# Kernel tuning notes

Measured on AMD Instinct MI355X. Metric: run time of the kernel, lower is better.

The kernel has to match this reference:

```python
import jax, jax.numpy as jnp
import numpy as np
import math

WS = 8       # window_size
NH = 4       # num_heads
D = 256      # d_model
B = 16
HH = 64
WW = 64
EPS = 1e-5


def _sincos_pe(ws, d):
    pe = np.zeros((ws * ws, d), np.float32)
    dh = d // 2
    y = np.repeat(np.arange(ws), ws).astype(np.float32)
    x = np.tile(np.arange(ws), ws).astype(np.float32)
    div = np.exp(np.arange(0, dh, 2).astype(np.float32) * (-math.log(10000.0) / dh))
    pe[:, 0:dh:2] = np.sin(y[:, None] * div)
    pe[:, 1:dh:2] = np.cos(y[:, None] * div)
    pe[:, dh::2] = np.sin(x[:, None] * div)
    pe[:, dh + 1::2] = np.cos(x[:, None] * div)
    return jnp.asarray(pe)[None]  # [1, ws*ws, d]


def setup_inputs() -> dict:
    key = jax.random.key(0)
    ks = iter(jax.random.split(key, 32))
    rnd = lambda *s: jax.random.normal(next(ks), s, dtype=jnp.float32) * 0.02
    inp = {
        'feat_A': jax.random.normal(next(ks), (B, HH * WW, D), dtype=jnp.float32),
        'feat_B': jax.random.normal(next(ks), (B, HH * WW, D), dtype=jnp.float32),
        'local_pe': _sincos_pe(WS, D),
    }
    for s in ('A', 'B'):
        inp[f'qkv_w_{s}'] = rnd(3, D, D)
        inp[f'qkv_b_{s}'] = rnd(3, D)
        inp[f'out_w_{s}'] = rnd(D, D)
        inp[f'out_b_{s}'] = rnd(D)
        inp[f'norm_g_{s}'] = jnp.ones((D,), jnp.float32)
        inp[f'norm_b_{s}'] = jnp.zeros((D,), jnp.float32)
        inp[f'ffn_norm_g_{s}'] = jnp.ones((D,), jnp.float32)
        inp[f'ffn_norm_b_{s}'] = jnp.zeros((D,), jnp.float32)
        inp[f'ffn_w1_{s}'] = rnd(2 * D, D)
        inp[f'ffn_b1_{s}'] = rnd(2 * D)
        inp[f'ffn_w2_{s}'] = rnd(D, 2 * D)
        inp[f'ffn_b2_{s}'] = rnd(D)
    inp['H'] = HH
    inp['W'] = WW
    return inp


def _partition(x, H, W):
    # [B, H*W, C] -> [B*nW, WS*WS, C]; H, W assumed divisible by WS (no pad branch)
    b, _, c = x.shape
    x = x.reshape(b, H // WS, WS, W // WS, WS, c)
    return x.transpose(0, 1, 3, 2, 4, 5).reshape(-1, WS * WS, c)


def _reverse(w, b, H, W):
    c = w.shape[-1]
    x = w.reshape(b, H // WS, W // WS, WS, WS, c)
    return x.transpose(0, 1, 3, 2, 4, 5).reshape(b, H * W, c)


def _ln(x, g, b):
    m = jnp.mean(x, -1, keepdims=True)
    v = jnp.mean(jnp.square(x - m), -1, keepdims=True)
    return (x - m) * jax.lax.rsqrt(v + EPS) * g + b


def _mha(q_in, kv_in, qkv_w, qkv_b, out_w, out_b):
    s, c = q_in.shape[1], q_in.shape[2]
    dh = c // NH
    q = (q_in @ qkv_w[0].T + qkv_b[0]).reshape(-1, s, NH, dh)
    k = (kv_in @ qkv_w[1].T + qkv_b[1]).reshape(-1, s, NH, dh)
    v = (kv_in @ qkv_w[2].T + qkv_b[2]).reshape(-1, s, NH, dh)
    attn = jax.nn.softmax(jnp.einsum('bqhd,bkhd->bhqk', q, k) / math.sqrt(dh), axis=-1)
    o = jnp.einsum('bhqk,bkhd->bqhd', attn, v).reshape(-1, s, c)
    return o @ out_w.T + out_b


def _ffn(x, w1, b1, w2, b2):
    return jax.nn.gelu(x @ w1.T + b1, approximate=False) @ w2.T + b2


def reference(feat_A, feat_B, local_pe,
              qkv_w_A, qkv_b_A, out_w_A, out_b_A,
              qkv_w_B, qkv_b_B, out_w_B, out_b_B,
              norm_g_A, norm_b_A, ffn_norm_g_A, ffn_norm_b_A,
              ffn_w1_A, ffn_b1_A, ffn_w2_A, ffn_b2_A,
              norm_g_B, norm_b_B, ffn_norm_g_B, ffn_norm_b_B,
              ffn_w1_B, ffn_b1_B, ffn_w2_B, ffn_b2_B,
              H, W):
    b = feat_A.shape[0]
    sc_A, sc_B = feat_A, feat_B
    win_A = _partition(feat_A, H, W) + local_pe
    win_B = _partition(feat_B, H, W) + local_pe
    attn_A = _mha(win_A, win_B, qkv_w_A, qkv_b_A, out_w_A, out_b_A)
    attn_B = _mha(win_B, win_A, qkv_w_B, qkv_b_B, out_w_B, out_b_B)
    fA = _reverse(attn_A, b, H, W)
    fB = _reverse(attn_B, b, H, W)
    fA = _ln(fA + sc_A, norm_g_A, norm_b_A)
    fA = _ln(fA + _ffn(fA, ffn_w1_A, ffn_b1_A, ffn_w2_A, ffn_b2_A), ffn_norm_g_A, ffn_norm_b_A)
    fB = _ln(fB + sc_B, norm_g_B, norm_b_B)
    fB = _ln(fB + _ffn(fB, ffn_w1_B, ffn_b1_B, ffn_w2_B, ffn_b2_B), ffn_norm_g_B, ffn_norm_b_B)
    return (fA, fB)
```

## Files before the change

### kernel.cpp

```cpp
#include <hip/hip_runtime.h>
#include <hip/hip_bf16.h>
#include <math.h>

typedef __bf16 bf16;
typedef __bf16 bf16x8 __attribute__((ext_vector_type(8)));
typedef __bf16 bf16x4 __attribute__((ext_vector_type(4)));
typedef float f32x4 __attribute__((ext_vector_type(4)));

#define NTOK 65536
#define DMODEL 256

#define GL16(g, l) __builtin_amdgcn_global_load_lds( \
    (const __attribute__((address_space(1))) void*)(g), \
    (__attribute__((address_space(3))) void*)(l), 16, 0, 0)

__device__ __forceinline__ int unwin_idx(int m) {
    int widx = m >> 6, t = m & 63;
    int b = widx >> 6, wl = widx & 63;
    return (b << 12) | (((wl >> 3) * 8 + (t >> 3)) << 6) | ((wl & 7) * 8 + (t & 7));
}

__device__ __forceinline__ float gelu_fast(float x) {
    float z = 0.7978845608f * (x + 0.044715f * x * x * x);
    float e = __expf(2.f * z);
    float t = (e - 1.f) / (e + 1.f);
    return 0.5f * x * (1.f + t);
}

__global__ __launch_bounds__(256)
void prep_win(const float* __restrict__ fA, const float* __restrict__ fB,
              const float* __restrict__ pe,
              bf16* __restrict__ awA, bf16* __restrict__ awB)
{
    const float* f = blockIdx.y ? fB : fA;
    bf16* aw = blockIdx.y ? awB : awA;
    int m = blockIdx.x * 8 + (threadIdx.x >> 5);
    int c = (threadIdx.x & 31) * 8;
    int g = unwin_idx(m), t = m & 63;
    const float4* fs = reinterpret_cast<const float4*>(f + (size_t)g * 256 + c);
    const float4* ps = reinterpret_cast<const float4*>(pe + t * 256 + c);
    float4 a0 = fs[0], a1 = fs[1], p0 = ps[0], p1 = ps[1];
    bf16x8 o;
    o[0] = (bf16)(a0.x + p0.x); o[1] = (bf16)(a0.y + p0.y);
    o[2] = (bf16)(a0.z + p0.z); o[3] = (bf16)(a0.w + p0.w);
    o[4] = (bf16)(a1.x + p1.x); o[5] = (bf16)(a1.y + p1.y);
    o[6] = (bf16)(a1.z + p1.z); o[7] = (bf16)(a1.w + p1.w);
    *reinterpret_cast<bf16x8*>(aw + (size_t)m * 256 + c) = o;
}

__global__ __launch_bounds__(256)
void cvt8(const float* __restrict__ s0, const float* __restrict__ s1,
          const float* __restrict__ s2, const float* __restrict__ s3,
          const float* __restrict__ s4, const float* __restrict__ s5,
          const float* __restrict__ s6, const float* __restrict__ s7,
          bf16* __restrict__ d)
{
    int idx = (blockIdx.x * 256 + threadIdx.x) * 4;
    const float* s; int off;
    if      (idx < 196608) { s = s0; off = 0; }
    else if (idx < 262144) { s = s1; off = 196608; }
    else if (idx < 393216) { s = s2; off = 262144; }
    else if (idx < 524288) { s = s3; off = 393216; }
    else if (idx < 720896) { s = s4; off = 524288; }
    else if (idx < 786432) { s = s5; off = 720896; }
    else if (idx < 917504) { s = s6; off = 786432; }
    else                   { s = s7; off = 917504; }
    float4 v = *reinterpret_cast<const float4*>(s + (idx - off));
    bf16x4 o; o[0] = (bf16)v.x; o[1] = (bf16)v.y; o[2] = (bf16)v.z; o[3] = (bf16)v.w;
    *reinterpret_cast<bf16x4*>(d + idx) = o;
}

__global__ __launch_bounds__(256, 4)
void gemm_qkv2(const bf16* __restrict__ awA, const bf16* __restrict__ awB,
               const bf16* __restrict__ wA, const bf16* __restrict__ wB,
               const float* __restrict__ bA, const float* __restrict__ bB,
               bf16* __restrict__ qA, bf16* __restrict__ kA, bf16* __restrict__ vA,
               bf16* __restrict__ qB, bf16* __restrict__ kB, bf16* __restrict__ vB)
{
    __shared__ bf16 As[2][4096];
    __shared__ bf16 Bs[2][4096];
    const int tid = threadIdx.x;
    const int bx = blockIdx.x;
    const int xcd = bx & 7, slot = bx >> 3;
    const int L = xcd * 768 + slot;
    const int mt = L / 6, nb = L - mt * 6;
    const int pass = mt >> 9, mb = mt & 511;
    const int seg = nb >> 1, nl0 = (nb & 1) * 128;
    const int m0 = mb * 128;

    const bf16* A = pass ? awB : awA;
    const bf16* Wf = (seg == 0) ? (pass ? wB : wA) : (pass ? wA : wB);
    const float* Bf = (seg == 0) ? (pass ? bB : bA) : (pass ? bA : bB);
    const bf16* W = Wf + (size_t)seg * 65536;
    const float* bia = Bf + seg * 256;
    bf16* qout = pass ? qB : qA;
    bf16* kout = pass ? kA : kB;
    bf16* vout = pass ? vA : vB;

    const int lane = tid & 63, w = tid >> 6;
    const int wr = w >> 1, wc = w & 1;
    const int lr = lane & 15, lg = lane >> 4;
    const int srow = tid >> 2, scol = (tid & 3) * 8;

    const bf16* Ag = A + (size_t)(m0 + srow) * 256 + scol;
    const bf16* Bg = W + (size_t)(nl0 + srow) * 256 + scol;

    f32x4 acc[4][4];
    const f32x4 zero = {0.f, 0.f, 0.f, 0.f};
#pragma unroll
    for (int mi = 0; mi < 4; ++mi)
#pragma unroll
        for (int nj = 0; nj < 4; ++nj) acc[mi][nj] = zero;

    auto stage = [&](int buf, int k0) {
        GL16(Ag + k0, &As[buf][tid * 8]);
        GL16(Ag + 64 * 256 + k0, &As[buf][2048 + tid * 8]);
        GL16(Bg + k0, &Bs[buf][tid * 8]);
        GL16(Bg + 64 * 256 + k0, &Bs[buf][2048 + tid * 8]);
    };
    auto compute = [&](int buf) {
        bf16x8 af[4], bfr[4];
#pragma unroll
        for (int mi = 0; mi < 4; ++mi)
            af[mi] = *reinterpret_cast<const bf16x8*>(&As[buf][(wr * 64 + mi * 16 + lr) * 32 + lg * 8]);
#pragma unroll
        for (int nj = 0; nj < 4; ++nj)
            bfr[nj] = *reinterpret_cast<const bf16x8*>(&Bs[buf][(wc * 64 + nj * 16 + lr) * 32 + lg * 8]);
#pragma unroll
        for (int mi = 0; mi < 4; ++mi)
#pragma unroll
            for (int nj = 0; nj < 4; ++nj)
                acc[mi][nj] = __builtin_amdgcn_mfma_f32_16x16x32_bf16(af[mi], bfr[nj], acc[mi][nj], 0, 0, 0);
    };

    stage(0, 0);
    __syncthreads();
#pragma unroll
    for (int t = 0; t < 7; ++t) {
        stage((t + 1) & 1, (t + 1) * 32);
        compute(t & 1);
        __syncthreads();
    }
    compute(1);

    if (seg == 2) {
        const int widx = mb * 2 + wr;
#pragma unroll
        for (int nj = 0; nj < 4; ++nj) {
            int cl = nl0 + wc * 64 + nj * 16 + lr;
            float bv = bia[cl];
#pragma unroll
            for (int mi = 0; mi < 4; ++mi) {
                bf16x4 o;
#pragma unroll
                for (int i = 0; i < 4; ++i) o[i] = (bf16)(acc[mi][nj][i] + bv);
                *reinterpret_cast<bf16x4*>(vout + ((size_t)widx * 256 + cl) * 64 + mi * 16 + lg * 4) = o;
            }
        }
    } else {
        bf16* out = (seg == 0) ? qout : kout;
#pragma unroll
        for (int nj = 0; nj < 4; ++nj) {
            int cl = nl0 + wc * 64 + nj * 16 + lr;
            float bv = bia[cl];
#pragma unroll
            for (int mi = 0; mi < 4; ++mi)
#pragma unroll
                for (int i = 0; i < 4; ++i) {
                    int row = m0 + wr * 64 + mi * 16 + lg * 4 + i;
                    out[(size_t)row * 256 + cl] = (bf16)(acc[mi][nj][i] + bv);
                }
        }
    }
}

__global__ __launch_bounds__(256, 4)
void gemm_gelu(const bf16* __restrict__ y1A, const bf16* __restrict__ y1B,
               const bf16* __restrict__ wA, const bf16* __restrict__ wB,
               const float* __restrict__ bA, const float* __restrict__ bB,
               bf16* __restrict__ hbA, bf16* __restrict__ hbB)
{
    __shared__ bf16 lds[17408];
    bf16* As = lds;
    bf16* Bs = lds + 8192;
    const int tid = threadIdx.x;
    const int bx = blockIdx.x;
    const int xcd = bx & 7, slot = bx >> 3;
    const int L = xcd * 512 + slot;
    const int mt = L >> 2, nb = L & 3;
    const int str = mt >> 9, mb = mt & 511;
    const int m0 = mb * 128, n0 = nb * 128;

    const bf16* A = str ? y1B : y1A;
    const bf16* W = str ? wB : wA;
    const float* bia = str ? bB : bA;
    bf16* C = str ? hbB : hbA;

    const int lane = tid & 63, w = tid >> 6;
    const int wr = w >> 1, wc = w & 1;
    const int lr = lane & 15, lg = lane >> 4;
    const int srow = tid >> 2, scol = (tid & 3) * 8;

    const bf16* Ag = A + (size_t)(m0 + srow) * 256 + scol;
    const bf16* Bg = W + (size_t)(n0 + srow) * 256 + scol;

    f32x4 acc[4][4];
    const f32x4 zero = {0.f, 0.f, 0.f, 0.f};
#pragma unroll
    for (int mi = 0; mi < 4; ++mi)
#pragma unroll
        for (int nj = 0; nj < 4; ++nj) acc[mi][nj] = zero;

    auto stage = [&](int buf, int k0) {
        GL16(Ag + k0, &As[buf * 4096 + tid * 8]);
        GL16(Ag + 64 * 256 + k0, &As[buf * 4096 + 2048 + tid * 8]);
        GL16(Bg + k0, &Bs[buf * 4096 + tid * 8]);
        GL16(Bg + 64 * 256 + k0, &Bs[buf * 4096 + 2048 + tid * 8]);
    };
    auto compute = [&](int buf) {
        bf16x8 af[4], bfr[4];
#pragma unroll
        for (int mi = 0; mi < 4; ++mi)
            af[mi] = *reinterpret_cast<const bf16x8*>(&As[buf * 4096 + (wr * 64 + mi * 16 + lr) * 32 + lg * 8]);
#pragma unroll
        for (int nj = 0; nj < 4; ++nj)
            bfr[nj] = *reinterpret_cast<const bf16x8*>(&Bs[buf * 4096 + (wc * 64 + nj * 16 + lr) * 32 + lg * 8]);
#pragma unroll
        for (int mi = 0; mi < 4; ++mi)
#pragma unroll
            for (int nj = 0; nj < 4; ++nj)
                acc[mi][nj] = __builtin_amdgcn_mfma_f32_16x16x32_bf16(af[mi], bfr[nj], acc[mi][nj], 0, 0, 0);
    };

    stage(0, 0);
    __syncthreads();
#pragma unroll
    for (int t = 0; t < 7; ++t) {
        stage((t + 1) & 1, (t + 1) * 32);
        compute(t & 1);
        __syncthreads();
    }
    compute(1);

    __syncthreads();
#pragma unroll
    for (int nj = 0; nj < 4; ++nj) {
        int coll = wc * 64 + nj * 16 + lr;
        float bv = bia[n0 + coll];
#pragma unroll
        for (int mi = 0; mi < 4; ++mi)
#pragma unroll
            for (int i = 0; i < 4; ++i) {
                int rowl = wr * 64 + mi * 16 + lg * 4 + i;
                lds[rowl * 136 + coll] = (bf16)gelu_fast(acc[mi][nj][i] + bv);
            }
    }
    __syncthreads();
#pragma unroll
    for (int j = 0; j < 4; ++j)
#pragma unroll
        for (int h = 0; h < 2; ++h) {
            int rowl = j * 32 + (tid >> 3);
            int coll = h * 64 + (tid & 7) * 8;
            *reinterpret_cast<bf16x8*>(C + (size_t)(m0 + rowl) * 512 + n0 + coll) =
                *reinterpret_cast<const bf16x8*>(&lds[rowl * 136 + coll]);
        }
}

template<int WK, int UNWIN>
__global__ __launch_bounds__(256, 4)
void gemm_out(const bf16* __restrict__ A0, const bf16* __restrict__ A1,
              const bf16* __restrict__ W0, const bf16* __restrict__ W1,
              const float* __restrict__ b0, const float* __restrict__ b1,
              bf16* __restrict__ C0, bf16* __restrict__ C1)
{
    __shared__ bf16 lds[17408];
    bf16* As = lds;
    bf16* Bs = lds + 8192;
    const int tid = threadIdx.x;
    const int bx = blockIdx.x;
    const int xcd = bx & 7, slot = bx >> 3;
    const int L = xcd * 256 + slot;
    const int mt = L >> 1, nb = L & 1;
    const int str = mt >> 9, mb = mt & 511;
    const int m0 = mb * 128, n0 = nb * 128;

    const bf16* A = str ? A1 : A0;
    const bf16* W = str ? W1 : W0;
    const float* bia = str ? b1 : b0;
    bf16* C = str ? C1 : C0;

    const int lane = tid & 63, w = tid >> 6;
    const int wr = w >> 1, wc = w & 1;
    const int lr = lane & 15, lg = lane >> 4;
    const int srow = tid >> 2, scol = (tid & 3) * 8;

    const bf16* Ag = A + (size_t)(m0 + srow) * WK + scol;
    const bf16* Bg = W + (size_t)(n0 + srow) * WK + scol;

    f32x4 acc[4][4];
    const f32x4 zero = {0.f, 0.f, 0.f, 0.f};
#pragma unroll
    for (int mi = 0; mi < 4; ++mi)
#pragma unroll
        for (int nj = 0; nj < 4; ++nj) acc[mi][nj] = zero;

    auto stage = [&](int buf, int k0) {
        GL16(Ag + k0, &As[buf * 4096 + tid * 8]);
        GL16(Ag + (size_t)64 * WK + k0, &As[buf * 4096 + 2048 + tid * 8]);
        GL16(Bg + k0, &Bs[buf * 4096 + tid * 8]);
        GL16(Bg + (size_t)64 * WK + k0, &Bs[buf * 4096 + 2048 + tid * 8]);
    };
    auto compute = [&](int buf) {
        bf16x8 af[4], bfr[4];
#pragma unroll
        for (int mi = 0; mi < 4; ++mi)
            af[mi] = *reinterpret_cast<const bf16x8*>(&As[buf * 4096 + (wr * 64 + mi * 16 + lr) * 32 + lg * 8]);
#pragma unroll
        for (int nj = 0; nj < 4; ++nj)
            bfr[nj] = *reinterpret_cast<const bf16x8*>(&Bs[buf * 4096 + (wc * 64 + nj * 16 + lr) * 32 + lg * 8]);
#pragma unroll
        for (int mi = 0; mi < 4; ++mi)
#pragma unroll
            for (int nj = 0; nj < 4; ++nj)
                acc[mi][nj] = __builtin_amdgcn_mfma_f32_16x16x32_bf16(af[mi], bfr[nj], acc[mi][nj], 0, 0, 0);
    };

    const int NT = WK / 32;
    stage(0, 0);
    __syncthreads();
#pragma unroll
    for (int t = 0; t < NT - 1; ++t) {
        stage((t + 1) & 1, (t + 1) * 32);
        compute(t & 1);
        __syncthreads();
    }
    compute((NT - 1) & 1);

    __syncthreads();
#pragma unroll
    for (int nj = 0; nj < 4; ++nj) {
        int coll = wc * 64 + nj * 16 + lr;
        float bv = bia[n0 + coll];
#pragma unroll
        for (int mi = 0; mi < 4; ++mi)
#pragma unroll
            for (int i = 0; i < 4; ++i) {
                int rowl = wr * 64 + mi * 16 + lg * 4 + i;
                lds[rowl * 136 + coll] = (bf16)(acc[mi][nj][i] + bv);
            }
    }
    __syncthreads();
#pragma unroll
    for (int j = 0; j < 4; ++j) {
        int rowl = j * 32 + (tid >> 3);
        int gr = UNWIN ? unwin_idx(m0 + rowl) : (m0 + rowl);
#pragma unroll
        for (int h = 0; h < 2; ++h) {
            int coll = h * 64 + (tid & 7) * 8;
            *reinterpret_cast<bf16x8*>(C + (size_t)gr * 256 + n0 + coll) =
                *reinterpret_cast<const bf16x8*>(&lds[rowl * 136 + coll]);
        }
    }
}

template<int RESF, int OUTF>
__global__ __launch_bounds__(256)
void ln_fz(const bf16* __restrict__ x0, const bf16* __restrict__ x1,
           const float* __restrict__ rf0, const float* __restrict__ rf1,
           const bf16* __restrict__ rb0, const bf16* __restrict__ rb1,
           const float* __restrict__ g0, const float* __restrict__ g1,
           const float* __restrict__ be0, const float* __restrict__ be1,
           float* __restrict__ of0, float* __restrict__ of1,
           bf16* __restrict__ ob0, bf16* __restrict__ ob1)
{
    const int bx = blockIdx.x;
    const int str = bx >> 14, b = bx & 16383;
    const bf16* x = str ? x1 : x0;
    const float* rf = str ? rf1 : rf0;
    const bf16* rb = str ? rb1 : rb0;
    const float* gamma = str ? g1 : g0;
    const float* beta = str ? be1 : be0;
    float* outf = str ? of1 : of0;
    bf16* outb = str ? ob1 : ob0;

    int row = b * 4 + (threadIdx.x >> 6);
    int lane = threadIdx.x & 63;
    size_t base = (size_t)row * 256 + lane * 4;
    bf16x4 xv = *reinterpret_cast<const bf16x4*>(x + base);
    float v[4];
    if (RESF) {
        float4 rv = *reinterpret_cast<const float4*>(rf + base);
        v[0] = rv.x + (float)xv[0];
        v[1] = rv.y + (float)xv[1];
        v[2] = rv.z + (float)xv[2];
        v[3] = rv.w + (float)xv[3];
    } else {
        bf16x4 rv = *reinterpret_cast<const bf16x4*>(rb + base);
        v[0] = (float)rv[0] + (float)xv[0];
        v[1] = (float)rv[1] + (float)xv[1];
        v[2] = (float)rv[2] + (float)xv[2];
        v[3] = (float)rv[3] + (float)xv[3];
    }
    float s = v[0] + v[1] + v[2] + v[3];
    float q = v[0] * v[0] + v[1] * v[1] + v[2] * v[2] + v[3] * v[3];
#pragma unroll
    for (int m = 1; m < 64; m <<= 1) {
        s += __shfl_xor(s, m);
        q += __shfl_xor(q, m);
    }
    float mean = s * (1.f / 256.f);
    float var = q * (1.f / 256.f) - mean * mean;
    float rstd = rsqrtf(var + 1e-5f);
    float4 gv = *reinterpret_cast<const float4*>(gamma + lane * 4);
    float4 bv = *reinterpret_cast<const float4*>(beta + lane * 4);
    float o[4];
    o[0] = (v[0] - mean) * rstd * gv.x + bv.x;
    o[1] = (v[1] - mean) * rstd * gv.y + bv.y;
    o[2] = (v[2] - mean) * rstd * gv.z + bv.z;
    o[3] = (v[3] - mean) * rstd * gv.w + bv.w;
    if (OUTF) {
        float4 ov; ov.x = o[0]; ov.y = o[1]; ov.z = o[2]; ov.w = o[3];
        *reinterpret_cast<float4*>(outf + base) = ov;
    } else {
        bf16x4 ob;
        ob[0] = (bf16)o[0]; ob[1] = (bf16)o[1]; ob[2] = (bf16)o[2]; ob[3] = (bf16)o[3];
        *reinterpret_cast<bf16x4*>(outb + base) = ob;
    }
}

__global__ __launch_bounds__(256)
void attn_win2(const bf16* qA, const bf16* __restrict__ kA,
               const bf16* __restrict__ vA,
               const bf16* qB, const bf16* __restrict__ kB,
               const bf16* __restrict__ vB)
{
    __shared__ bf16 Ps[4][64][72];
    const int tid = threadIdx.x;
    const int wv = tid >> 6, lane = tid & 63;
    const int str = blockIdx.x >> 10, widx = blockIdx.x & 1023, head = wv;
    const int lr = lane & 15, lg = lane >> 4;
    const bf16* qbuf = str ? qB : qA;
    const bf16* kbuf = str ? kB : kA;
    const bf16* vtbuf = str ? vB : vA;
    bf16* obuf = const_cast<bf16*>(qbuf);
    const bf16* qb = qbuf + (size_t)widx * 64 * 256 + head * 64;
    const bf16* kb = kbuf + (size_t)widx * 64 * 256 + head * 64;
    const bf16* vb = vtbuf + (size_t)widx * 16384 + head * 64 * 64;

    const f32x4 zero = {0.f, 0.f, 0.f, 0.f};
    f32x4 sacc[4][4];
#pragma unroll
    for (int mi = 0; mi < 4; ++mi)
#pragma unroll
        for (int nj = 0; nj < 4; ++nj) sacc[mi][nj] = zero;

#pragma unroll
    for (int k0 = 0; k0 < 64; k0 += 32) {
        bf16x8 af[4], bfr[4];
#pragma unroll
        for (int mi = 0; mi < 4; ++mi)
            af[mi] = *reinterpret_cast<const bf16x8*>(qb + (size_t)(mi * 16 + lr) * 256 + k0 + lg * 8);
#pragma unroll
        for (int nj = 0; nj < 4; ++nj)
            bfr[nj] = *reinterpret_cast<const bf16x8*>(kb + (size_t)(nj * 16 + lr) * 256 + k0 + lg * 8);
#pragma unroll
        for (int mi = 0; mi < 4; ++mi)
#pragma unroll
            for (int nj = 0; nj < 4; ++nj)
                sacc[mi][nj] = __builtin_amdgcn_mfma_f32_16x16x32_bf16(af[mi], bfr[nj], sacc[mi][nj], 0, 0, 0);
    }

    const float c = 0.125f * 1.4426950408889634f;
    float rsum[4][4];
#pragma unroll
    for (int mi = 0; mi < 4; ++mi)
#pragma unroll
        for (int i = 0; i < 4; ++i) {
            float m = fmaxf(fmaxf(sacc[mi][0][i], sacc[mi][1][i]), fmaxf(sacc[mi][2][i], sacc[mi][3][i]));
            m = fmaxf(m, __shfl_xor(m, 1));
            m = fmaxf(m, __shfl_xor(m, 2));
            m = fmaxf(m, __shfl_xor(m, 4));
            m = fmaxf(m, __shfl_xor(m, 8));
#pragma unroll
            for (int nj = 0; nj < 4; ++nj)
                sacc[mi][nj][i] = exp2f((sacc[mi][nj][i] - m) * c);
            float s = sacc[mi][0][i] + sacc[mi][1][i] + sacc[mi][2][i] + sacc[mi][3][i];
            s += __shfl_xor(s, 1);
            s += __shfl_xor(s, 2);
            s += __shfl_xor(s, 4);
            s += __shfl_xor(s, 8);
            rsum[mi][i] = s;
        }

#pragma unroll
    for (int mi = 0; mi < 4; ++mi)
#pragma unroll
        for (int nj = 0; nj < 4; ++nj)
#pragma unroll
            for (int i = 0; i < 4; ++i)
                Ps[wv][mi * 16 + lg * 4 + i][nj * 16 + lr] = (bf16)sacc[mi][nj][i];

    f32x4 oacc[4][4];
#pragma unroll
    for (int mi = 0; mi < 4; ++mi)
#pragma unroll
        for (int nj = 0; nj < 4; ++nj) oacc[mi][nj] = zero;
#pragma unroll
    for (int k0 = 0; k0 < 64; k0 += 32) {
        bf16x8 af[4], bfr[4];
#pragma unroll
        for (int mi = 0; mi < 4; ++mi)
            af[mi] = *reinterpret_cast<const bf16x8*>(&Ps[wv][mi * 16 + lr][k0 + lg * 8]);
#pragma unroll
        for (int nj = 0; nj < 4; ++nj)
            bfr[nj] = *reinterpret_cast<const bf16x8*>(vb + (size_t)(nj * 16 + lr) * 64 + k0 + lg * 8);
#pragma unroll
        for (int mi = 0; mi < 4; ++mi)
#pragma unroll
            for (int nj = 0; nj < 4; ++nj)
                oacc[mi][nj] = __builtin_amdgcn_mfma_f32_16x16x32_bf16(af[mi], bfr[nj], oacc[mi][nj], 0, 0, 0);
    }
#pragma unroll
    for (int mi = 0; mi < 4; ++mi)
#pragma unroll
        for (int i = 0; i < 4; ++i) {
            float inv = 1.0f / rsum[mi][i];
            int row = mi * 16 + lg * 4 + i;
#pragma unroll
            for (int nj = 0; nj < 4; ++nj)
                obuf[((size_t)widx * 64 + row) * 256 + head * 64 + nj * 16 + lr] =
                    (bf16)(oacc[mi][nj][i] * inv);
        }
}

extern "C" void kernel_launch(void* const* d_in, const int* in_sizes, int n_in,
                              void* d_out, int out_size, void* d_ws, size_t ws_size,
                              hipStream_t stream)
{
    const float* feat_A       = (const float*)d_in[0];
    const float* feat_B       = (const float*)d_in[1];
    const float* pe           = (const float*)d_in[2];
    const float* qkv_w_A      = (const float*)d_in[3];
    const float* qkv_b_A      = (const float*)d_in[4];
    const float* out_w_A      = (const float*)d_in[5];
    const float* out_b_A      = (const float*)d_in[6];
    const float* norm_g_A     = (const float*)d_in[7];
    const float* norm_b_A     = (const float*)d_in[8];
    const float* ffn_norm_g_A = (const float*)d_in[9];
    const float* ffn_norm_b_A = (const float*)d_in[10];
    const float* ffn_w1_A     = (const float*)d_in[11];
    const float* ffn_b1_A     = (const float*)d_in[12];
    const float* ffn_w2_A     = (const float*)d_in[13];
    const float* ffn_b2_A     = (const float*)d_in[14];
    const float* qkv_w_B      = (const float*)d_in[15];
    const float* qkv_b_B      = (const float*)d_in[16];
    const float* out_w_B      = (const float*)d_in[17];
    const float* out_b_B      = (const float*)d_in[18];
    const float* norm_g_B     = (const float*)d_in[19];
    const float* norm_b_B     = (const float*)d_in[20];
    const float* ffn_norm_g_B = (const float*)d_in[21];
    const float* ffn_norm_b_B = (const float*)d_in[22];
    const float* ffn_w1_B     = (const float*)d_in[23];
    const float* ffn_b1_B     = (const float*)d_in[24];
    const float* ffn_w2_B     = (const float*)d_in[25];
    const float* ffn_b2_B     = (const float*)d_in[26];

    char* ws = (char*)d_ws;
    const size_t BFE = (size_t)NTOK * 256;
    const size_t BFB = BFE * 2;

    bf16* Wb = (bf16*)ws;
    size_t off = 2u * 1024 * 1024;
    bf16* awA = (bf16*)(ws + off); off += BFB;
    bf16* awB = (bf16*)(ws + off); off += BFB;
    bf16* qA  = (bf16*)(ws + off); off += BFB;
    bf16* kA  = (bf16*)(ws + off); off += BFB;
    bf16* vA  = (bf16*)(ws + off); off += BFB;
    bf16* qB  = (bf16*)(ws + off); off += BFB;
    bf16* kB  = (bf16*)(ws + off); off += BFB;
    bf16* vB  = (bf16*)(ws + off); off += BFB;
    bf16* tb1A = kA;
    bf16* tb1B = vA;
    bf16* y1A = kB;
    bf16* y1B = vB;
    bf16* hbA = awA;
    bf16* hbB = kA;
    bf16* tb2A = qA;
    bf16* tb2B = qB;

    bf16* w_qkvA = Wb + 0;
    bf16* w_outA = Wb + 196608;
    bf16* w_f1A  = Wb + 262144;
    bf16* w_f2A  = Wb + 393216;
    bf16* w_qkvB = Wb + 524288;
    bf16* w_outB = Wb + 720896;
    bf16* w_f1B  = Wb + 786432;
    bf16* w_f2B  = Wb + 917504;

    cvt8<<<1024, 256, 0, stream>>>(qkv_w_A, out_w_A, ffn_w1_A, ffn_w2_A,
                                   qkv_w_B, out_w_B, ffn_w1_B, ffn_w2_B, Wb);
    prep_win<<<dim3(8192, 2), 256, 0, stream>>>(feat_A, feat_B, pe, awA, awB);

    gemm_qkv2<<<6144, 256, 0, stream>>>(awA, awB, w_qkvA, w_qkvB,
                                        qkv_b_A, qkv_b_B,
                                        qA, kA, vA, qB, kB, vB);

    attn_win2<<<2048, 256, 0, stream>>>(qA, kA, vA, qB, kB, vB);

    gemm_out<256, 1><<<2048, 256, 0, stream>>>(qA, qB, w_outA, w_outB,
                                               out_b_A, out_b_B, tb1A, tb1B);
    ln_fz<1, 0><<<32768, 256, 0, stream>>>(tb1A, tb1B, feat_A, feat_B,
                                           nullptr, nullptr,
                                           norm_g_A, norm_g_B, norm_b_A, norm_b_B,
                                           nullptr, nullptr, y1A, y1B);
    gemm_gelu<<<4096, 256, 0, stream>>>(y1A, y1B, w_f1A, w_f1B,
                                        ffn_b1_A, ffn_b1_B, hbA, hbB);
    gemm_out<512, 0><<<2048, 256, 0, stream>>>(hbA, hbB, w_f2A, w_f2B,
                                               ffn_b2_A, ffn_b2_B, tb2A, tb2B);
    ln_fz<0, 1><<<32768, 256, 0, stream>>>(tb2A, tb2B, nullptr, nullptr,
                                           y1A, y1B,
                                           ffn_norm_g_A, ffn_norm_g_B,
                                           ffn_norm_b_A, ffn_norm_b_B,
                                           (float*)d_out, (float*)d_out + BFE,
                                           nullptr, nullptr);
}
```

Baseline: 455.2 us.

## Fuse window partition and PE add into QKV GEMM A-load; stage Q/K stores via LDS

Removes the prep_win kernel and has the QKV GEMM read fp32 features directly, gather them through the window index, add the positional encoding and convert to bf16 while writing a padded LDS tile. This drops the intermediate bf16 window buffers, saving a full write and read of them. The fp32 A tile is now read six times, once per N-block, instead of the smaller bf16 copy, and the loads are synchronous rather than async global-to-LDS. Separately, Q/K outputs are staged through LDS so they can be written with coalesced 16-byte stores instead of scalar scattered bf16 stores.

```diff
diff --git a/kernel.cpp b/kernel.cpp
--- a/kernel.cpp
+++ b/kernel.cpp
@@ -25,27 +25,6 @@
     float e = __expf(2.f * z);
     float t = (e - 1.f) / (e + 1.f);
     return 0.5f * x * (1.f + t);
-}
-
-__global__ __launch_bounds__(256)
-void prep_win(const float* __restrict__ fA, const float* __restrict__ fB,
-              const float* __restrict__ pe,
-              bf16* __restrict__ awA, bf16* __restrict__ awB)
-{
-    const float* f = blockIdx.y ? fB : fA;
-    bf16* aw = blockIdx.y ? awB : awA;
-    int m = blockIdx.x * 8 + (threadIdx.x >> 5);
-    int c = (threadIdx.x & 31) * 8;
-    int g = unwin_idx(m), t = m & 63;
-    const float4* fs = reinterpret_cast<const float4*>(f + (size_t)g * 256 + c);
-    const float4* ps = reinterpret_cast<const float4*>(pe + t * 256 + c);
-    float4 a0 = fs[0], a1 = fs[1], p0 = ps[0], p1 = ps[1];
-    bf16x8 o;
-    o[0] = (bf16)(a0.x + p0.x); o[1] = (bf16)(a0.y + p0.y);
-    o[2] = (bf16)(a0.z + p0.z); o[3] = (bf16)(a0.w + p0.w);
-    o[4] = (bf16)(a1.x + p1.x); o[5] = (bf16)(a1.y + p1.y);
-    o[6] = (bf16)(a1.z + p1.z); o[7] = (bf16)(a1.w + p1.w);
-    *reinterpret_cast<bf16x8*>(aw + (size_t)m * 256 + c) = o;
 }
 
 __global__ __launch_bounds__(256)
@@ -71,14 +50,16 @@
 }
 
 __global__ __launch_bounds__(256, 4)
-void gemm_qkv2(const bf16* __restrict__ awA, const bf16* __restrict__ awB,
+void gemm_qkvf(const float* __restrict__ feat_A, const float* __restrict__ feat_B,
+               const float* __restrict__ pe,
                const bf16* __restrict__ wA, const bf16* __restrict__ wB,
                const float* __restrict__ bA, const float* __restrict__ bB,
                bf16* __restrict__ qA, bf16* __restrict__ kA, bf16* __restrict__ vA,
                bf16* __restrict__ qB, bf16* __restrict__ kB, bf16* __restrict__ vB)
 {
-    __shared__ bf16 As[2][4096];
-    __shared__ bf16 Bs[2][4096];
+    __shared__ bf16 lds[18432];
+    bf16* As = lds;
+    bf16* Bs = lds + 10240;
     const int tid = threadIdx.x;
     const int bx = blockIdx.x;
     const int xcd = bx & 7, slot = bx >> 3;
@@ -88,7 +69,7 @@
     const int seg = nb >> 1, nl0 = (nb & 1) * 128;
     const int m0 = mb * 128;
 
-    const bf16* A = pass ? awB : awA;
+    const float* feat = pass ? feat_B : feat_A;
     const bf16* Wf = (seg == 0) ? (pass ? wB : wA) : (pass ? wA : wB);
     const float* Bf = (seg == 0) ? (pass ? bB : bA) : (pass ? bA : bB);
     const bf16* W = Wf + (size_t)seg * 65536;
@@ -101,8 +82,14 @@
     const int wr = w >> 1, wc = w & 1;
     const int lr = lane & 15, lg = lane >> 4;
     const int srow = tid >> 2, scol = (tid & 3) * 8;
-
-    const bf16* Ag = A + (size_t)(m0 + srow) * 256 + scol;
+    const int r = tid >> 1, cs = (tid & 1) * 16;
+
+    const int mrow = m0 + r;
+    const int tA = mrow & 63;
+    const int gA = unwin_idx(mrow);
+    const float* fsrc = feat + (size_t)gA * DMODEL + cs;
+    const float* psrc = pe + tA * DMODEL + cs;
+
     const bf16* Bg = W + (size_t)(nl0 + srow) * 256 + scol;
 
     f32x4 acc[4][4];
@@ -112,20 +99,31 @@
 #pragma unroll
         for (int nj = 0; nj < 4; ++nj) acc[mi][nj] = zero;
 
-    auto stage = [&](int buf, int k0) {
-        GL16(Ag + k0, &As[buf][tid * 8]);
-        GL16(Ag + 64 * 256 + k0, &As[buf][2048 + tid * 8]);
-        GL16(Bg + k0, &Bs[buf][tid * 8]);
-        GL16(Bg + 64 * 256 + k0, &Bs[buf][2048 + tid * 8]);
+    auto stageB = [&](int buf, int k0) {
+        GL16(Bg + k0, &Bs[buf * 4096 + tid * 8]);
+        GL16(Bg + 64 * 256 + k0, &Bs[buf * 4096 + 2048 + tid * 8]);
+    };
+    auto stageA = [&](int buf, int k0) {
+        const float4* fs = reinterpret_cast<const float4*>(fsrc + k0);
+        const float4* ps = reinterpret_cast<const float4*>(psrc + k0);
+        bf16* dst = &As[buf * 5120 + r * 40 + cs];
+#pragma unroll
+        for (int q = 0; q < 4; ++q) {
+            float4 a = fs[q], p = ps[q];
+            dst[q * 4 + 0] = (bf16)(a.x + p.x);
+            dst[q * 4 + 1] = (bf16)(a.y + p.y);
+            dst[q * 4 + 2] = (bf16)(a.z + p.z);
+            dst[q * 4 + 3] = (bf16)(a.w + p.w);
+        }
     };
     auto compute = [&](int buf) {
         bf16x8 af[4], bfr[4];
 #pragma unroll
         for (int mi = 0; mi < 4; ++mi)
-            af[mi] = *reinterpret_cast<const bf16x8*>(&As[buf][(wr * 64 + mi * 16 + lr) * 32 + lg * 8]);
+            af[mi] = *reinterpret_cast<const bf16x8*>(&As[buf * 5120 + (wr * 64 + mi * 16 + lr) * 40 + lg * 8]);
 #pragma unroll
         for (int nj = 0; nj < 4; ++nj)
-            bfr[nj] = *reinterpret_cast<const bf16x8*>(&Bs[buf][(wc * 64 + nj * 16 + lr) * 32 + lg * 8]);
+            bfr[nj] = *reinterpret_cast<const bf16x8*>(&Bs[buf * 4096 + (wc * 64 + nj * 16 + lr) * 32 + lg * 8]);
 #pragma unroll
         for (int mi = 0; mi < 4; ++mi)
 #pragma unroll
@@ -133,11 +131,13 @@
                 acc[mi][nj] = __builtin_amdgcn_mfma_f32_16x16x32_bf16(af[mi], bfr[nj], acc[mi][nj], 0, 0, 0);
     };
 
-    stage(0, 0);
+    stageB(0, 0);
+    stageA(0, 0);
     __syncthreads();
 #pragma unroll
     for (int t = 0; t < 7; ++t) {
-        stage((t + 1) & 1, (t + 1) * 32);
+        stageB((t + 1) & 1, (t + 1) * 32);
+        stageA((t + 1) & 1, (t + 1) * 32);
         compute(t & 1);
         __syncthreads();
     }
@@ -159,17 +159,29 @@
         }
     } else {
         bf16* out = (seg == 0) ? qout : kout;
+        __syncthreads();
 #pragma unroll
         for (int nj = 0; nj < 4; ++nj) {
-            int cl = nl0 + wc * 64 + nj * 16 + lr;
-            float bv = bia[cl];
+            int coll = wc * 64 + nj * 16 + lr;
+            float bv = bia[nl0 + coll];
 #pragma unroll
             for (int mi = 0; mi < 4; ++mi)
 #pragma unroll
                 for (int i = 0; i < 4; ++i) {
-                    int row = m0 + wr * 64 + mi * 16 + lg * 4 + i;
-                    out[(size_t)row * 256 + cl] = (bf16)(acc[mi][nj][i] + bv);
+                    int rowl = wr * 64 + mi * 16 + lg * 4 + i;
+                    lds[rowl * 136 + coll] = (bf16)(acc[mi][nj][i] + bv);
                 }
+        }
+        __syncthreads();
+#pragma unroll
+        for (int j = 0; j < 4; ++j) {
+            int rowl = j * 32 + (tid >> 3);
+#pragma unroll
+            for (int h = 0; h < 2; ++h) {
+                int coll = h * 64 + (tid & 7) * 8;
+                *reinterpret_cast<bf16x8*>(out + (size_t)(m0 + rowl) * 256 + nl0 + coll) =
+                    *reinterpret_cast<const bf16x8*>(&lds[rowl * 136 + coll]);
+            }
         }
     }
 }
@@ -600,9 +612,8 @@
 
     cvt8<<<1024, 256, 0, stream>>>(qkv_w_A, out_w_A, ffn_w1_A, ffn_w2_A,
                                    qkv_w_B, out_w_B, ffn_w1_B, ffn_w2_B, Wb);
-    prep_win<<<dim3(8192, 2), 256, 0, stream>>>(feat_A, feat_B, pe, awA, awB);
-
-    gemm_qkv2<<<6144, 256, 0, stream>>>(awA, awB, w_qkvA, w_qkvB,
+
+    gemm_qkvf<<<6144, 256, 0, stream>>>(feat_A, feat_B, pe, w_qkvA, w_qkvB,
                                         qkv_b_A, qkv_b_B,
                                         qA, kA, vA, qB, kB, vB);
 
```

Measured after the change: 493.7 us. 8.5% more time.

## Fuse FFN up-projection, GELU and down-projection into one kernel

Applied to the files above, without the earlier changes.

Replaces the separate GELU GEMM and second FFN GEMM with a single kernel that computes each 128-column hidden chunk into LDS and immediately accumulates it into the down-projection. This removes writing and rereading the 512-wide hidden activation to global memory and one kernel launch. It uses 512-thread blocks with larger LDS, so each block holds more registers (two accumulator sets) and occupancy drops. W1 is reloaded per block and several extra barriers are added per chunk.

```diff
diff --git a/kernel.cpp b/kernel.cpp
--- a/kernel.cpp
+++ b/kernel.cpp
@@ -174,97 +174,153 @@
     }
 }
 
-__global__ __launch_bounds__(256, 4)
-void gemm_gelu(const bf16* __restrict__ y1A, const bf16* __restrict__ y1B,
-               const bf16* __restrict__ wA, const bf16* __restrict__ wB,
-               const float* __restrict__ bA, const float* __restrict__ bB,
-               bf16* __restrict__ hbA, bf16* __restrict__ hbB)
-{
-    __shared__ bf16 lds[17408];
-    bf16* As = lds;
-    bf16* Bs = lds + 8192;
+__global__ __launch_bounds__(512, 2)
+void gemm_ffn(const bf16* __restrict__ y1A, const bf16* __restrict__ y1B,
+              const bf16* __restrict__ w1A, const bf16* __restrict__ w1B,
+              const bf16* __restrict__ w2A, const bf16* __restrict__ w2B,
+              const float* __restrict__ b1A, const float* __restrict__ b1B,
+              const float* __restrict__ b2A, const float* __restrict__ b2B,
+              bf16* __restrict__ tb2A, bf16* __restrict__ tb2B)
+{
+    __shared__ bf16 lds[33792];
+    bf16* Hs = lds + 16384;
     const int tid = threadIdx.x;
     const int bx = blockIdx.x;
-    const int xcd = bx & 7, slot = bx >> 3;
-    const int L = xcd * 512 + slot;
-    const int mt = L >> 2, nb = L & 3;
-    const int str = mt >> 9, mb = mt & 511;
-    const int m0 = mb * 128, n0 = nb * 128;
-
-    const bf16* A = str ? y1B : y1A;
-    const bf16* W = str ? wB : wA;
-    const float* bia = str ? bB : bA;
-    bf16* C = str ? hbB : hbA;
-
-    const int lane = tid & 63, w = tid >> 6;
-    const int wr = w >> 1, wc = w & 1;
+    const int L = (bx & 7) * 128 + (bx >> 3);
+    const int str = L >> 9, mb = L & 511;
+    const int m0 = mb * 128;
+
+    const bf16* Y  = str ? y1B : y1A;
+    const bf16* W1 = str ? w1B : w1A;
+    const bf16* W2 = str ? w2B : w2A;
+    const float* b1 = str ? b1B : b1A;
+    const float* b2 = str ? b2B : b2A;
+    bf16* out = str ? tb2B : tb2A;
+
+    const int w = tid >> 6, lane = tid & 63;
+    const int wr = w >> 2, wc = w & 3;
     const int lr = lane & 15, lg = lane >> 4;
     const int srow = tid >> 2, scol = (tid & 3) * 8;
 
-    const bf16* Ag = A + (size_t)(m0 + srow) * 256 + scol;
-    const bf16* Bg = W + (size_t)(n0 + srow) * 256 + scol;
-
-    f32x4 acc[4][4];
+    const bf16* Yg  = Y + (size_t)(m0 + srow) * 256 + scol;
+    const bf16* W2g = W2 + (size_t)srow * 512 + scol;
+
+    f32x4 acc2[4][4];
     const f32x4 zero = {0.f, 0.f, 0.f, 0.f};
 #pragma unroll
     for (int mi = 0; mi < 4; ++mi)
 #pragma unroll
-        for (int nj = 0; nj < 4; ++nj) acc[mi][nj] = zero;
-
-    auto stage = [&](int buf, int k0) {
-        GL16(Ag + k0, &As[buf * 4096 + tid * 8]);
-        GL16(Ag + 64 * 256 + k0, &As[buf * 4096 + 2048 + tid * 8]);
-        GL16(Bg + k0, &Bs[buf * 4096 + tid * 8]);
-        GL16(Bg + 64 * 256 + k0, &Bs[buf * 4096 + 2048 + tid * 8]);
-    };
-    auto compute = [&](int buf) {
-        bf16x8 af[4], bfr[4];
-#pragma unroll
-        for (int mi = 0; mi < 4; ++mi)
-            af[mi] = *reinterpret_cast<const bf16x8*>(&As[buf * 4096 + (wr * 64 + mi * 16 + lr) * 32 + lg * 8]);
-#pragma unroll
-        for (int nj = 0; nj < 4; ++nj)
-            bfr[nj] = *reinterpret_cast<const bf16x8*>(&Bs[buf * 4096 + (wc * 64 + nj * 16 + lr) * 32 + lg * 8]);
-#pragma unroll
-        for (int mi = 0; mi < 4; ++mi)
+        for (int nj = 0; nj < 4; ++nj) acc2[mi][nj] = zero;
+
+    for (int nb = 0; nb < 4; ++nb) {
+        const bf16* W1g = W1 + (size_t)(nb * 128 + srow) * 256 + scol;
+        f32x4 acc1[4][2];
+#pragma unroll
+        for (int mi = 0; mi < 4; ++mi)
+#pragma unroll
+            for (int nj = 0; nj < 2; ++nj) acc1[mi][nj] = zero;
+
+        auto stage1 = [&](int buf, int k0) {
+            GL16(Yg + k0,  &lds[buf * 4096 + tid * 8]);
+            GL16(W1g + k0, &lds[8192 + buf * 4096 + tid * 8]);
+        };
+        auto compute1 = [&](int buf) {
+            bf16x8 af[4], bfr[2];
+#pragma unroll
+            for (int mi = 0; mi < 4; ++mi)
+                af[mi] = *reinterpret_cast<const bf16x8*>(&lds[buf * 4096 + (wr * 64 + mi * 16 + lr) * 32 + lg * 8]);
+#pragma unroll
+            for (int nj = 0; nj < 2; ++nj)
+                bfr[nj] = *reinterpret_cast<const bf16x8*>(&lds[8192 + buf * 4096 + (wc * 32 + nj * 16 + lr) * 32 + lg * 8]);
+#pragma unroll
+            for (int mi = 0; mi < 4; ++mi)
+#pragma unroll
+                for (int nj = 0; nj < 2; ++nj)
+                    acc1[mi][nj] = __builtin_amdgcn_mfma_f32_16x16x32_bf16(af[mi], bfr[nj], acc1[mi][nj], 0, 0, 0);
+        };
+
+        stage1(0, 0);
+        __syncthreads();
+#pragma unroll
+        for (int t = 0; t < 7; ++t) {
+            stage1((t + 1) & 1, (t + 1) * 32);
+            compute1(t & 1);
+            __syncthreads();
+        }
+        compute1(1);
+
+#pragma unroll
+        for (int nj = 0; nj < 2; ++nj) {
+            int col = wc * 32 + nj * 16 + lr;
+            float bv = b1[nb * 128 + col];
+#pragma unroll
+            for (int mi = 0; mi < 4; ++mi)
+#pragma unroll
+                for (int i = 0; i < 4; ++i) {
+                    int row = wr * 64 + mi * 16 + lg * 4 + i;
+                    Hs[row * 136 + col] = (bf16)gelu_fast(acc1[mi][nj][i] + bv);
+                }
+        }
+        __syncthreads();
+
+        auto stage2 = [&](int buf, int k0) {
+            GL16(W2g + nb * 128 + k0, &lds[buf * 8192 + tid * 8]);
+            GL16(W2g + 128 * 512 + nb * 128 + k0, &lds[buf * 8192 + 4096 + tid * 8]);
+        };
+        auto compute2 = [&](int buf, int k0) {
+            bf16x8 af[4], bfr[4];
+#pragma unroll
+            for (int mi = 0; mi < 4; ++mi)
+                af[mi] = *reinterpret_cast<const bf16x8*>(&Hs[(wr * 64 + mi * 16 + lr) * 136 + k0 + lg * 8]);
 #pragma unroll
             for (int nj = 0; nj < 4; ++nj)
-                acc[mi][nj] = __builtin_amdgcn_mfma_f32_16x16x32_bf16(af[mi], bfr[nj], acc[mi][nj], 0, 0, 0);
-    };
-
-    stage(0, 0);
-    __syncthreads();
-#pragma unroll
-    for (int t = 0; t < 7; ++t) {
-        stage((t + 1) & 1, (t + 1) * 32);
-        compute(t & 1);
-        __syncthreads();
-    }
-    compute(1);
-
-    __syncthreads();
-#pragma unroll
-    for (int nj = 0; nj < 4; ++nj) {
-        int coll = wc * 64 + nj * 16 + lr;
-        float bv = bia[n0 + coll];
-#pragma unroll
-        for (int mi = 0; mi < 4; ++mi)
-#pragma unroll
-            for (int i = 0; i < 4; ++i) {
-                int rowl = wr * 64 + mi * 16 + lg * 4 + i;
-                lds[rowl * 136 + coll] = (bf16)gelu_fast(acc[mi][nj][i] + bv);
+                bfr[nj] = *reinterpret_cast<const bf16x8*>(&lds[buf * 8192 + (wc * 64 + nj * 16 + lr) * 32 + lg * 8]);
+#pragma unroll
+            for (int mi = 0; mi < 4; ++mi)
+#pragma unroll
+                for (int nj = 0; nj < 4; ++nj)
+                    acc2[mi][nj] = __builtin_amdgcn_mfma_f32_16x16x32_bf16(af[mi], bfr[nj], acc2[mi][nj], 0, 0, 0);
+        };
+
+        stage2(0, 0);
+        __syncthreads();
+#pragma unroll
+        for (int t = 0; t < 3; ++t) {
+            stage2((t + 1) & 1, (t + 1) * 32);
+            compute2(t & 1, t * 32);
+            __syncthreads();
+        }
+        compute2(1, 96);
+        __syncthreads();
+    }
+
+#pragma unroll
+    for (int h = 0; h < 2; ++h) {
+        if ((wc >> 1) == h) {
+#pragma unroll
+            for (int nj = 0; nj < 4; ++nj) {
+                int colw = nj * 16 + lr;
+                float bv = b2[wc * 64 + colw];
+                int coll = (wc & 1) * 64 + colw;
+#pragma unroll
+                for (int mi = 0; mi < 4; ++mi)
+#pragma unroll
+                    for (int i = 0; i < 4; ++i) {
+                        int row = wr * 64 + mi * 16 + lg * 4 + i;
+                        Hs[row * 136 + coll] = (bf16)(acc2[mi][nj][i] + bv);
+                    }
             }
-    }
-    __syncthreads();
-#pragma unroll
-    for (int j = 0; j < 4; ++j)
-#pragma unroll
-        for (int h = 0; h < 2; ++h) {
-            int rowl = j * 32 + (tid >> 3);
-            int coll = h * 64 + (tid & 7) * 8;
-            *reinterpret_cast<bf16x8*>(C + (size_t)(m0 + rowl) * 512 + n0 + coll) =
-                *reinterpret_cast<const bf16x8*>(&lds[rowl * 136 + coll]);
-        }
+        }
+        __syncthreads();
+#pragma unroll
+        for (int j = 0; j < 4; ++j) {
+            int rowl = j * 32 + (tid >> 4);
+            int coll = (tid & 15) * 8;
+            *reinterpret_cast<bf16x8*>(out + (size_t)(m0 + rowl) * 256 + h * 128 + coll) =
+                *reinterpret_cast<const bf16x8*>(&Hs[rowl * 136 + coll]);
+        }
+        __syncthreads();
+    }
 }
 
 template<int WK, int UNWIN>
@@ -584,8 +640,6 @@
     bf16* tb1B = vA;
     bf16* y1A = kB;
     bf16* y1B = vB;
-    bf16* hbA = awA;
-    bf16* hbB = kA;
     bf16* tb2A = qA;
     bf16* tb2B = qB;
 
@@ -614,10 +668,9 @@
                                            nullptr, nullptr,
                                            norm_g_A, norm_g_B, norm_b_A, norm_b_B,
                                            nullptr, nullptr, y1A, y1B);
-    gemm_gelu<<<4096, 256, 0, stream>>>(y1A, y1B, w_f1A, w_f1B,
-                                        ffn_b1_A, ffn_b1_B, hbA, hbB);
-    gemm_out<512, 0><<<2048, 256, 0, stream>>>(hbA, hbB, w_f2A, w_f2B,
-                                               ffn_b2_A, ffn_b2_B, tb2A, tb2B);
+    gemm_ffn<<<1024, 512, 0, stream>>>(y1A, y1B, w_f1A, w_f1B, w_f2A, w_f2B,
+                                       ffn_b1_A, ffn_b1_B, ffn_b2_A, ffn_b2_B,
+                                       tb2A, tb2B);
     ln_fz<0, 1><<<32768, 256, 0, stream>>>(tb2A, tb2B, nullptr, nullptr,
                                            y1A, y1B,
                                            ffn_norm_g_A, ffn_norm_g_B,
```

New measurement: 481.9 us. 5.9% more time.
